# Performance work log

Measured on AMD Instinct MI355X. Metric: run time of the kernel, lower is better.

Reference implementation:

```python
import jax, jax.numpy as jnp
import numpy as np

HEADS = 4
HID = 610
KER = 50  # cov2KerSize
NEG_SLOPE = 0.2


def gat_layer(x, src, dst, w, b, att_src, att_dst, n_nodes):
    # x: [N, Fin], w: [HEADS*HID, Fin], att_*: [1, HEADS, HID], b: [HID]
    h = (x @ w.T).reshape(n_nodes, HEADS, HID)               # [N,H,D]
    a_src = (h * att_src).sum(-1)                            # [N,H]
    a_dst = (h * att_dst).sum(-1)                            # [N,H]
    alpha = jax.nn.leaky_relu(a_src[src] + a_dst[dst], NEG_SLOPE)  # [E,H]
    # softmax over edges grouped by destination node
    m = jax.ops.segment_max(alpha, dst, num_segments=n_nodes)
    e = jnp.exp(alpha - m[dst])
    denom = jax.ops.segment_sum(e, dst, num_segments=n_nodes)
    a = e / (denom[dst] + 1e-16)                             # [E,H]
    msg = h[src] * a[:, :, None]                             # [E,H,D]
    out = jax.ops.segment_sum(msg, dst, num_segments=n_nodes)  # [N,H,D]
    return out.mean(axis=1) + b                              # [N,D] (concat=False)


def setup_inputs() -> dict:
    key = jax.random.key(0)
    ks = jax.random.split(key, 16)
    N, E, FIN, NOUT = 20000, 100000, 128, 86
    x = jax.random.normal(ks[0], (N, FIN), dtype=jnp.float32)
    edge_index = jax.random.randint(ks[1], (2, E), 0, N, dtype=jnp.int64)
    def kaiming(k, shape, fan_in):
        return jax.random.normal(k, shape, dtype=jnp.float32) * np.float32(np.sqrt(2.0 / fan_in))
    w0 = kaiming(ks[2], (HEADS * HID, FIN), FIN)
    b0 = jnp.zeros((HID,), jnp.float32)
    att_src0 = kaiming(ks[3], (1, HEADS, HID), HID)
    att_dst0 = kaiming(ks[4], (1, HEADS, HID), HID)
    w2 = kaiming(ks[5], (HEADS * HID, HID), HID)
    b2 = jnp.zeros((HID,), jnp.float32)
    att_src1 = kaiming(ks[6], (1, HEADS, HID), HID)
    att_dst1 = kaiming(ks[7], (1, HEADS, HID), HID)
    w4 = kaiming(ks[8], (1, 1, 2, KER), 2 * KER)
    b4 = jnp.zeros((1,), jnp.float32)
    w6 = kaiming(ks[9], (1, 1, KER), KER)
    b6 = jnp.zeros((1,), jnp.float32)
    w8 = kaiming(ks[10], (NOUT, 512), 512)
    b8 = jnp.zeros((NOUT,), jnp.float32)
    return dict(x=x, edge_index=edge_index, w0=w0, b0=b0, att_src0=att_src0,
                att_dst0=att_dst0, w2=w2, b2=b2, att_src1=att_src1,
                att_dst1=att_dst1, w4=w4, b4=b4, w6=w6, b6=b6, w8=w8, b8=b8)


def reference(x, edge_index, w0, b0, att_src0, att_dst0, w2, b2, att_src1,
              att_dst1, w4, b4, w6, b6, w8, b8):
    N = x.shape[0]
    src, dst = edge_index[0], edge_index[1]
    x1 = jax.nn.relu(gat_layer(x, src, dst, w0, b0, att_src0, att_dst0, N))
    x2 = jax.nn.relu(gat_layer(x1, src, dst, w2, b2, att_src1, att_dst1, N))
    # edge features: cat(src_feat, dst_feat) viewed as [E,1,2,HID]
    ef = jnp.stack([x2[src], x2[dst]], axis=1)[:, None, :, :]  # [E,1,2,HID]
    y = jax.lax.conv_general_dilated(ef, w4, (1, 1), 'VALID',
                                     dimension_numbers=('NCHW', 'OIHW', 'NCHW'))
    y = jax.nn.relu(y + b4[None, :, None, None])               # [E,1,1,561]
    y = y.reshape(-1, HID - KER + 1, 1).transpose(0, 2, 1)     # [E,1,561]
    y = jax.lax.conv_general_dilated(y, w6, (1,), 'VALID',
                                     dimension_numbers=('NCH', 'OIH', 'NCH'))
    y = jax.nn.relu(y + b6[None, :, None])                     # [E,1,512]
    # adaptive_avg_pool1d to 512 is identity since length is already 512
    y = y.reshape(-1, 512)
    return y @ w8.T + b8                                       # [E, num_outputs]
```

## Files before the change

### kernel.cpp

```cpp
#include <hip/hip_runtime.h>
#include <math.h>

#define HEADS 4
#define HID 610
#define HIDP 640
#define FIN 128
#define KER 50
#define NOUT 86
#define NEG_SLOPE 0.2f

typedef short bf8_t __attribute__((ext_vector_type(8)));
typedef float f4_t __attribute__((ext_vector_type(4)));

__device__ __forceinline__ ushort f2bf(float f) {
    unsigned u = __float_as_uint(f);
    unsigned r = (u + 0x7FFFu + ((u >> 16) & 1u)) >> 16;
    return (ushort)r;
}
__device__ __forceinline__ float bf2f(ushort b) { return __uint_as_float(((unsigned)b) << 16); }

__global__ void fill_val(float* __restrict__ p, float v, long n) {
    long i = (long)blockIdx.x * blockDim.x + threadIdx.x;
    if (i < n) p[i] = v;
}

__global__ void copy_int(const int* __restrict__ a, int* __restrict__ b, int n) {
    int i = blockIdx.x * blockDim.x + threadIdx.x;
    if (i < n) b[i] = a[i];
}

__global__ void hist_k(const int* __restrict__ ei, int* __restrict__ hist, int E) {
    int e = blockIdx.x * blockDim.x + threadIdx.x;
    if (e < E) atomicAdd(&hist[ei[E + e]], 1);
}

__global__ __launch_bounds__(1024) void scan_k(const int* __restrict__ hist,
                                               int* __restrict__ base, int Nn) {
    __shared__ int tmp[1024];
    __shared__ int carry;
    if (threadIdx.x == 0) carry = 0;
    __syncthreads();
    for (int c0 = 0; c0 < Nn; c0 += 1024) {
        int i = c0 + threadIdx.x;
        int v = (i < Nn) ? hist[i] : 0;
        tmp[threadIdx.x] = v;
        __syncthreads();
        for (int off = 1; off < 1024; off <<= 1) {
            int t = (threadIdx.x >= off) ? tmp[threadIdx.x - off] : 0;
            __syncthreads();
            tmp[threadIdx.x] += t;
            __syncthreads();
        }
        if (i < Nn) base[i] = carry + tmp[threadIdx.x] - v;
        __syncthreads();
        if (threadIdx.x == 1023) carry += tmp[1023];
        __syncthreads();
    }
    if (threadIdx.x == 0) base[Nn] = carry;
}

__global__ void scatter_k(const int* __restrict__ ei, int* __restrict__ cursor,
                          int* __restrict__ esrc, int E) {
    int e = blockIdx.x * blockDim.x + threadIdx.x;
    if (e >= E) return;
    int d = ei[E + e];
    int pos = atomicAdd(&cursor[d], 1);
    esrc[pos] = ei[e];
}

__global__ void split_pad(const float* __restrict__ in, ushort* __restrict__ hi,
                          ushort* __restrict__ lo, int R, int K, int Kp) {
    long i = (long)blockIdx.x * blockDim.x + threadIdx.x;
    if (i >= (long)R * Kp) return;
    int r = (int)(i / Kp), c = (int)(i % Kp);
    float v = (c < K) ? in[(long)r * K + c] : 0.f;
    ushort h = f2bf(v);
    hi[i] = h;
    lo[i] = f2bf(v - bf2f(h));
}

template <int AMODE, bool BIAS>
__global__ __launch_bounds__(256) void gemm_mfma(const float* __restrict__ A,
                                                 const ushort* __restrict__ Aghi,
                                                 const ushort* __restrict__ Aglo,
                                                 const ushort* __restrict__ Bghi,
                                                 const ushort* __restrict__ Bglo,
                                                 const float* __restrict__ bias,
                                                 float* __restrict__ C,
                                                 int M, int N, int Kp) {
    __shared__ __align__(16) ushort Ah[128 * 32];
    __shared__ __align__(16) ushort Al[128 * 32];
    __shared__ __align__(16) ushort Bh[128 * 32];
    __shared__ __align__(16) ushort Bl[128 * 32];
    int tid = threadIdx.x;
    int wave = tid >> 6, lane = tid & 63;
    int quad = lane >> 4, l16 = lane & 15;
    int wm = wave & 1, wn = wave >> 1;
    int row0 = blockIdx.y * 128, col0 = blockIdx.x * 128;

    float4 pa0[4];
    uint4 pah[2], pal[2], pbh[2], pbl[2];

    auto loadA = [&](int k0) {
        if (AMODE == 0) {
#pragma unroll
            for (int q = 0; q < 4; q++) {
                int p = tid + q * 256;
                int r = p >> 3, c4 = (p & 7) << 2;
                int gr = row0 + r;
                pa0[q] = (gr < M) ? *(const float4*)(A + (size_t)gr * Kp + k0 + c4)
                                  : make_float4(0.f, 0.f, 0.f, 0.f);
            }
        } else {
#pragma unroll
            for (int q = 0; q < 2; q++) {
                int p = tid + q * 256;
                int r = p >> 2, c = p & 3;
                int gr = row0 + r;
                if (gr < M) {
                    pah[q] = *(const uint4*)(Aghi + (size_t)gr * Kp + k0 + c * 8);
                    pal[q] = *(const uint4*)(Aglo + (size_t)gr * Kp + k0 + c * 8);
                } else {
                    pah[q] = make_uint4(0, 0, 0, 0);
                    pal[q] = make_uint4(0, 0, 0, 0);
                }
            }
        }
    };
    auto loadB = [&](int k0) {
#pragma unroll
        for (int q = 0; q < 2; q++) {
            int p = tid + q * 256;
            int r = p >> 2, c = p & 3;
            int gr = col0 + r;
            if (gr < N) {
                pbh[q] = *(const uint4*)(Bghi + (size_t)gr * Kp + k0 + c * 8);
                pbl[q] = *(const uint4*)(Bglo + (size_t)gr * Kp + k0 + c * 8);
            } else {
                pbh[q] = make_uint4(0, 0, 0, 0);
                pbl[q] = make_uint4(0, 0, 0, 0);
            }
        }
    };
    auto writeLDS = [&]() {
        if (AMODE == 0) {
#pragma unroll
            for (int q = 0; q < 4; q++) {
                int p = tid + q * 256;
                int r = p >> 3, m = p & 7;
                int pos = r * 32 + ((((m >> 1)) ^ ((r >> 1) & 3)) << 3) + ((m & 1) << 2);
                float4 v = pa0[q];
                ushort4 hv, lv;
                hv.x = f2bf(v.x); lv.x = f2bf(v.x - bf2f(hv.x));
                hv.y = f2bf(v.y); lv.y = f2bf(v.y - bf2f(hv.y));
                hv.z = f2bf(v.z); lv.z = f2bf(v.z - bf2f(hv.z));
                hv.w = f2bf(v.w); lv.w = f2bf(v.w - bf2f(hv.w));
                *(ushort4*)&Ah[pos] = hv;
                *(ushort4*)&Al[pos] = lv;
            }
        } else {
#pragma unroll
            for (int q = 0; q < 2; q++) {
                int p = tid + q * 256;
                int r = p >> 2, c = p & 3;
                int pos = r * 32 + ((c ^ ((r >> 1) & 3)) << 3);
                *(uint4*)&Ah[pos] = pah[q];
                *(uint4*)&Al[pos] = pal[q];
            }
        }
#pragma unroll
        for (int q = 0; q < 2; q++) {
            int p = tid + q * 256;
            int r = p >> 2, c = p & 3;
            int pos = r * 32 + ((c ^ ((r >> 1) & 3)) << 3);
            *(uint4*)&Bh[pos] = pbh[q];
            *(uint4*)&Bl[pos] = pbl[q];
        }
    };

    f4_t acc[4][4];
#pragma unroll
    for (int i = 0; i < 4; i++)
#pragma unroll
        for (int j = 0; j < 4; j++) acc[i][j] = (f4_t){0.f, 0.f, 0.f, 0.f};

    loadA(0);
    loadB(0);
    int sw = (quad ^ ((l16 >> 1) & 3)) << 3;
    for (int k0 = 0; k0 < Kp; k0 += 32) {
        __syncthreads();
        writeLDS();
        __syncthreads();
        if (k0 + 32 < Kp) {
            loadA(k0 + 32);
            loadB(k0 + 32);
        }
        bf8_t ah[4], al[4], bh[4], bl[4];
#pragma unroll
        for (int t = 0; t < 4; t++) {
            int ar = wm * 64 + t * 16 + l16;
            ah[t] = *(const bf8_t*)&Ah[ar * 32 + sw];
            al[t] = *(const bf8_t*)&Al[ar * 32 + sw];
            int br = wn * 64 + t * 16 + l16;
            bh[t] = *(const bf8_t*)&Bh[br * 32 + sw];
            bl[t] = *(const bf8_t*)&Bl[br * 32 + sw];
        }
#pragma unroll
        for (int i = 0; i < 4; i++)
#pragma unroll
            for (int j = 0; j < 4; j++) {
                acc[i][j] = __builtin_amdgcn_mfma_f32_16x16x32_bf16(ah[i], bh[j], acc[i][j], 0, 0, 0);
                acc[i][j] = __builtin_amdgcn_mfma_f32_16x16x32_bf16(al[i], bh[j], acc[i][j], 0, 0, 0);
                acc[i][j] = __builtin_amdgcn_mfma_f32_16x16x32_bf16(ah[i], bl[j], acc[i][j], 0, 0, 0);
            }
    }
#pragma unroll
    for (int i = 0; i < 4; i++) {
#pragma unroll
        for (int r = 0; r < 4; r++) {
            int grow = row0 + wm * 64 + i * 16 + quad * 4 + r;
            if (grow >= M) continue;
#pragma unroll
            for (int j = 0; j < 4; j++) {
                int gcol = col0 + wn * 64 + j * 16 + l16;
                if (gcol >= N) continue;
                float v = acc[i][j][r];
                if (BIAS) v += bias[gcol];
                C[(size_t)grow * N + gcol] = v;
            }
        }
    }
}

__global__ __launch_bounds__(256) void attn_dots(const float* __restrict__ h,
                                                 const float* __restrict__ att_s,
                                                 const float* __restrict__ att_d,
                                                 float* __restrict__ a_src,
                                                 float* __restrict__ a_dst, int Nn) {
    int n = blockIdx.x;
    int head = threadIdx.x >> 6;
    int lane = threadIdx.x & 63;
    const float2* hr = (const float2*)(h + (long)n * (HEADS * HID) + head * HID);
    const float2* as = (const float2*)(att_s + head * HID);
    const float2* ad = (const float2*)(att_d + head * HID);
    float ss = 0.f, sd = 0.f;
    for (int d = lane; d < HID / 2; d += 64) {
        float2 hv = hr[d], av = as[d], dv = ad[d];
        ss += hv.x * av.x + hv.y * av.y;
        sd += hv.x * dv.x + hv.y * dv.y;
    }
    for (int off = 32; off > 0; off >>= 1) {
        ss += __shfl_down(ss, off);
        sd += __shfl_down(sd, off);
    }
    if (lane == 0) {
        a_src[n * HEADS + head] = ss;
        a_dst[n * HEADS + head] = sd;
    }
}

template <int OUTMODE>
__global__ __launch_bounds__(256) void node_aggregate(
    const float* __restrict__ h, const float* __restrict__ asrc,
    const float* __restrict__ adst, const int* __restrict__ base,
    const int* __restrict__ esrc, const float* __restrict__ bias,
    float* __restrict__ xout, ushort* __restrict__ xhi, ushort* __restrict__ xlo,
    int Nn) {
    int wave = threadIdx.x >> 6, lane = threadIdx.x & 63;
    int n = blockIdx.x * 4 + wave;
    if (n >= Nn) return;
    int b0 = base[n], deg = base[n + 1] - b0;
    float ad[HEADS];
#pragma unroll
    for (int hh = 0; hh < HEADS; hh++) ad[hh] = adst[n * HEADS + hh];
    float m[HEADS] = {-INFINITY, -INFINITY, -INFINITY, -INFINITY};
    for (int eb = 0; eb < deg; eb += 64) {
        int i = eb + lane;
        if (i < deg) {
            int s = esrc[b0 + i];
#pragma unroll
            for (int hh = 0; hh < HEADS; hh++) {
                float v = asrc[s * HEADS + hh] + ad[hh];
                v = v >= 0.f ? v : NEG_SLOPE * v;
                m[hh] = fmaxf(m[hh], v);
            }
        }
    }
#pragma unroll
    for (int off = 32; off > 0; off >>= 1)
#pragma unroll
        for (int hh = 0; hh < HEADS; hh++) m[hh] = fmaxf(m[hh], __shfl_xor(m[hh], off));
    float sden[HEADS] = {0.f, 0.f, 0.f, 0.f};
    for (int eb = 0; eb < deg; eb += 64) {
        int i = eb + lane;
        if (i < deg) {
            int s = esrc[b0 + i];
#pragma unroll
            for (int hh = 0; hh < HEADS; hh++) {
                float v = asrc[s * HEADS + hh] + ad[hh];
                v = v >= 0.f ? v : NEG_SLOPE * v;
                sden[hh] += expf(v - m[hh]);
            }
        }
    }
#pragma unroll
    for (int off = 32; off > 0; off >>= 1)
#pragma unroll
        for (int hh = 0; hh < HEADS; hh++) sden[hh] += __shfl_xor(sden[hh], off);
    float inv[HEADS];
#pragma unroll
    for (int hh = 0; hh < HEADS; hh++) inv[hh] = 0.25f / (sden[hh] + 1e-16f);
    float acc0[10] = {}, acc1[10] = {}, acc2[10] = {}, acc3[10] = {};
    for (int eb = 0; eb < deg; eb += 64) {
        int i = eb + lane;
        int sreg = 0;
        float coef[HEADS] = {0.f, 0.f, 0.f, 0.f};
        if (i < deg) {
            sreg = esrc[b0 + i];
#pragma unroll
            for (int hh = 0; hh < HEADS; hh++) {
                float v = asrc[sreg * HEADS + hh] + ad[hh];
                v = v >= 0.f ? v : NEG_SLOPE * v;
                coef[hh] = expf(v - m[hh]) * inv[hh];
            }
        }
        int cnt = deg - eb < 64 ? deg - eb : 64;
        for (int j = 0; j < cnt; j++) {
            int s = __shfl(sreg, j);
            float c0 = __shfl(coef[0], j), c1 = __shfl(coef[1], j);
            float c2 = __shfl(coef[2], j), c3 = __shfl(coef[3], j);
            const float* hr = h + (size_t)s * (HEADS * HID);
#pragma unroll
            for (int t = 0; t < 10; t++) {
                int d = lane + t * 64;
                if (d < HID) {
                    acc0[t] = fmaf(c0, hr[d], acc0[t]);
                    acc1[t] = fmaf(c1, hr[HID + d], acc1[t]);
                    acc2[t] = fmaf(c2, hr[2 * HID + d], acc2[t]);
                    acc3[t] = fmaf(c3, hr[3 * HID + d], acc3[t]);
                }
            }
        }
    }
#pragma unroll
    for (int t = 0; t < 10; t++) {
        int d = lane + t * 64;
        if (d < HID) {
            float v = acc0[t] + acc1[t] + acc2[t] + acc3[t] + bias[d];
            v = v > 0.f ? v : 0.f;
            if (OUTMODE == 0) {
                xout[(size_t)n * HIDP + d] = v;
            } else {
                ushort hv = f2bf(v);
                xhi[(size_t)n * HIDP + d] = hv;
                xlo[(size_t)n * HIDP + d] = f2bf(v - bf2f(hv));
            }
        }
    }
    for (int d = HID + lane; d < HIDP; d += 64) {
        if (OUTMODE == 0) {
            xout[(size_t)n * HIDP + d] = 0.f;
        } else {
            xhi[(size_t)n * HIDP + d] = 0;
            xlo[(size_t)n * HIDP + d] = 0;
        }
    }
}

__device__ __forceinline__ int ystag(int j) { return j + (j >> 3); }

__global__ __launch_bounds__(256) void edge_conv(const float* __restrict__ x2,
                                                 const int* __restrict__ ei,
                                                 const float* __restrict__ w4,
                                                 const float* __restrict__ b4,
                                                 const float* __restrict__ w6,
                                                 const float* __restrict__ b6,
                                                 ushort* __restrict__ zhi,
                                                 ushort* __restrict__ zlo, int E) {
    __shared__ __align__(16) float2 st[4][632];
    __shared__ __align__(16) float y[4][652];
    int wave = threadIdx.x >> 6;
    int lane = threadIdx.x & 63;
    int e = blockIdx.x * 4 + wave;
    bool active = (e < E);
    if (active) {
        int sidx = ei[e];
        int didx = ei[E + e];
        const float2* sp = (const float2*)(x2 + (long)sidx * HIDP);
        const float2* tp = (const float2*)(x2 + (long)didx * HIDP);
        for (int i = lane; i < HID / 2; i += 64) {
            float2 sv = sp[i], tv = tp[i];
            *(float4*)&st[wave][2 * i] = make_float4(sv.x, tv.x, sv.y, tv.y);
        }
    }
    __syncthreads();
    float bb4 = b4[0], bb6 = b6[0];
    if (active) {
        int j0 = lane * 9;
        float acc[9];
        float2 W[18];
#pragma unroll
        for (int i = 0; i < 9; i++) acc[i] = bb4;
#pragma unroll
        for (int p = 0; p < 18; p++) W[p] = st[wave][j0 + p];
#pragma unroll
        for (int g = 0; g < 6; g++) {
#pragma unroll
            for (int mm = 0; mm < 9; mm++) {
                int k = 9 * g + mm;
                if (k < KER) {
                    float ws_ = w4[k], wt_ = w4[KER + k];
#pragma unroll
                    for (int i = 0; i < 9; i++) {
                        float2 v = W[(9 * g + mm + i) % 18];
                        acc[i] = fmaf(v.x, ws_, acc[i]);
                        acc[i] = fmaf(v.y, wt_, acc[i]);
                    }
                }
            }
            if (g < 5) {
#pragma unroll
                for (int p = 0; p < 9; p++)
                    W[(9 * g + p) % 18] = st[wave][j0 + 9 * g + 18 + p];
            }
        }
#pragma unroll
        for (int i = 0; i < 9; i++)
            y[wave][ystag(j0 + i)] = acc[i] > 0.f ? acc[i] : 0.f;
    }
    __syncthreads();
    if (active) {
        int j0 = lane * 8;
        float acc[8];
        float Y[16];
#pragma unroll
        for (int i = 0; i < 8; i++) acc[i] = bb6;
#pragma unroll
        for (int p = 0; p < 16; p++) Y[p] = y[wave][ystag(j0 + p)];
#pragma unroll
        for (int g = 0; g < 7; g++) {
#pragma unroll
            for (int mm = 0; mm < 8; mm++) {
                int k = 8 * g + mm;
                if (k < KER) {
                    float wv = w6[k];
#pragma unroll
                    for (int i = 0; i < 8; i++)
                        acc[i] = fmaf(Y[(8 * g + mm + i) % 16], wv, acc[i]);
                }
            }
            if (g < 6) {
#pragma unroll
                for (int p = 0; p < 8; p++)
                    Y[(8 * g + p) % 16] = y[wave][ystag(j0 + 8 * g + 16 + p)];
            }
        }
        ushort4 zh0, zh1, zl0, zl1;
        float v;
        v = acc[0] > 0.f ? acc[0] : 0.f; zh0.x = f2bf(v); zl0.x = f2bf(v - bf2f(zh0.x));
        v = acc[1] > 0.f ? acc[1] : 0.f; zh0.y = f2bf(v); zl0.y = f2bf(v - bf2f(zh0.y));
        v = acc[2] > 0.f ? acc[2] : 0.f; zh0.z = f2bf(v); zl0.z = f2bf(v - bf2f(zh0.z));
        v = acc[3] > 0.f ? acc[3] : 0.f; zh0.w = f2bf(v); zl0.w = f2bf(v - bf2f(zh0.w));
        v = acc[4] > 0.f ? acc[4] : 0.f; zh1.x = f2bf(v); zl1.x = f2bf(v - bf2f(zh1.x));
        v = acc[5] > 0.f ? acc[5] : 0.f; zh1.y = f2bf(v); zl1.y = f2bf(v - bf2f(zh1.y));
        v = acc[6] > 0.f ? acc[6] : 0.f; zh1.z = f2bf(v); zl1.z = f2bf(v - bf2f(zh1.z));
        v = acc[7] > 0.f ? acc[7] : 0.f; zh1.w = f2bf(v); zl1.w = f2bf(v - bf2f(zh1.w));
        size_t zo = (size_t)e * 512 + j0;
        *(ushort4*)&zhi[zo] = zh0;
        *(ushort4*)&zhi[zo + 4] = zh1;
        *(ushort4*)&zlo[zo] = zl0;
        *(ushort4*)&zlo[zo + 4] = zl1;
    }
}

extern "C" void kernel_launch(void* const* d_in, const int* in_sizes, int n_in,
                              void* d_out, int out_size, void* d_ws, size_t ws_size,
                              hipStream_t stream) {
    const float* x = (const float*)d_in[0];
    const int* ei = (const int*)d_in[1];
    const float* w0 = (const float*)d_in[2];
    const float* b0 = (const float*)d_in[3];
    const float* att_s0 = (const float*)d_in[4];
    const float* att_d0 = (const float*)d_in[5];
    const float* w2 = (const float*)d_in[6];
    const float* b2 = (const float*)d_in[7];
    const float* att_s1 = (const float*)d_in[8];
    const float* att_d1 = (const float*)d_in[9];
    const float* w4 = (const float*)d_in[10];
    const float* b4 = (const float*)d_in[11];
    const float* w6 = (const float*)d_in[12];
    const float* b6 = (const float*)d_in[13];
    const float* w8 = (const float*)d_in[14];
    const float* b8 = (const float*)d_in[15];
    float* out = (float*)d_out;

    const int Nn = in_sizes[0] / FIN;
    const int E = in_sizes[1] / 2;
    const int HD = HEADS * HID;

    float* ws = (float*)d_ws;
    size_t o = 0;
    float* buf1 = ws + o; o += (size_t)Nn * HIDP;
    ushort* x1hi = (ushort*)buf1;
    ushort* x1lo = x1hi + (size_t)Nn * HIDP;
    ushort* w8hi = (ushort*)(ws + o);
    ushort* w8lo = w8hi + (size_t)NOUT * 512; o += (size_t)NOUT * 512;
    ushort* zhi = (ushort*)(ws + o);
    ushort* zlo = zhi + (size_t)E * 512;
    int* base = (int*)(ws + o); o += (size_t)Nn + 4;
    int* cursor = (int*)(ws + o); o += (size_t)Nn;
    int* esrc = (int*)(ws + o); o += (size_t)E;
    float* asrc = ws + o; o += (size_t)Nn * HEADS;
    float* adst = ws + o; o += (size_t)Nn * HEADS;
    ushort* w0hi = (ushort*)(ws + o);
    ushort* w0lo = w0hi + (size_t)HD * FIN; o += (size_t)HD * FIN;
    ushort* w2hi = (ushort*)(ws + o);
    ushort* w2lo = w2hi + (size_t)HD * HIDP; o += (size_t)HD * HIDP;
    float* h = ws + o;

    int edgeGrid = (E + 255) / 256;
    int nodeWaveGrid = (Nn + 3) / 4;
    int edgeConvGrid = (E + 3) / 4;
    dim3 gGemmL((HD + 127) / 128, (Nn + 127) / 128);
    dim3 gGemmF((NOUT + 127) / 128, (E + 127) / 128);

    split_pad<<<((HD * FIN) + 255) / 256, 256, 0, stream>>>(w0, w0hi, w0lo, HD, FIN, FIN);
    split_pad<<<((HD * HIDP) + 255) / 256, 256, 0, stream>>>(w2, w2hi, w2lo, HD, HID, HIDP);
    split_pad<<<((NOUT * 512) + 255) / 256, 256, 0, stream>>>(w8, w8hi, w8lo, NOUT, 512, 512);
    fill_val<<<(Nn + 255) / 256, 256, 0, stream>>>((float*)cursor, 0.f, Nn);
    hist_k<<<edgeGrid, 256, 0, stream>>>(ei, cursor, E);
    scan_k<<<1, 1024, 0, stream>>>(cursor, base, Nn);
    copy_int<<<(Nn + 255) / 256, 256, 0, stream>>>(base, cursor, Nn);
    scatter_k<<<edgeGrid, 256, 0, stream>>>(ei, cursor, esrc, E);

    gemm_mfma<0, false><<<gGemmL, 256, 0, stream>>>(x, nullptr, nullptr, w0hi, w0lo, nullptr,
                                                    h, Nn, HD, FIN);
    attn_dots<<<Nn, 256, 0, stream>>>(h, att_s0, att_d0, asrc, adst, Nn);
    node_aggregate<1><<<nodeWaveGrid, 256, 0, stream>>>(h, asrc, adst, base, esrc, b0,
                                                        nullptr, x1hi, x1lo, Nn);

    gemm_mfma<1, false><<<gGemmL, 256, 0, stream>>>(nullptr, x1hi, x1lo, w2hi, w2lo, nullptr,
                                                    h, Nn, HD, HIDP);
    attn_dots<<<Nn, 256, 0, stream>>>(h, att_s1, att_d1, asrc, adst, Nn);
    node_aggregate<0><<<nodeWaveGrid, 256, 0, stream>>>(h, asrc, adst, base, esrc, b2,
                                                        buf1, nullptr, nullptr, Nn);

    edge_conv<<<edgeConvGrid, 256, 0, stream>>>(buf1, ei, w4, b4, w6, b6, zhi, zlo, E);

    gemm_mfma<1, true><<<gGemmF, 256, 0, stream>>>(nullptr, zhi, zlo, w8hi, w8lo, b8,
                                                   out, E, NOUT, 512);
}
```

Before: 1.124 ms.

## Fold attention vectors into weights and vectorize node aggregation loads

Precomputes U = W^T·att per head so the attention logits come from a small GEMV on the layer input (x or x1) rather than a pass over the full h tensor. This removes the read of the large N×2440 h matrix in each attention-dot kernel. Node aggregation also switches to float2 loads and stores. The reassociated dot product changes floating-point rounding slightly, and compute_u runs serial per-thread loops over HID.

Result: slower. 1.210 ms (+7.6%).

```diff
diff --git a/kernel.cpp b/kernel.cpp
--- a/kernel.cpp
+++ b/kernel.cpp
@@ -77,6 +77,22 @@
     ushort h = f2bf(v);
     hi[i] = h;
     lo[i] = f2bf(v - bf2f(h));
+}
+
+__global__ void compute_u(const float* __restrict__ w, const float* __restrict__ att_s,
+                          const float* __restrict__ att_d, float* __restrict__ U,
+                          int K, int Kp) {
+    int gid = blockIdx.x * blockDim.x + threadIdx.x;
+    if (gid >= Kp * 8) return;
+    int k = gid % Kp, c = gid / Kp;
+    int h = c & 3;
+    const float* att = (c < 4) ? att_s : att_d;
+    float acc = 0.f;
+    if (k < K) {
+        for (int d = 0; d < HID; d++)
+            acc += w[((size_t)(h * HID + d)) * K + k] * att[h * HID + d];
+    }
+    U[k * 8 + c] = acc;
 }
 
 template <int AMODE, bool BIAS>
@@ -232,30 +248,74 @@
     }
 }
 
-__global__ __launch_bounds__(256) void attn_dots(const float* __restrict__ h,
-                                                 const float* __restrict__ att_s,
-                                                 const float* __restrict__ att_d,
-                                                 float* __restrict__ a_src,
-                                                 float* __restrict__ a_dst, int Nn) {
-    int n = blockIdx.x;
-    int head = threadIdx.x >> 6;
-    int lane = threadIdx.x & 63;
-    const float2* hr = (const float2*)(h + (long)n * (HEADS * HID) + head * HID);
-    const float2* as = (const float2*)(att_s + head * HID);
-    const float2* ad = (const float2*)(att_d + head * HID);
-    float ss = 0.f, sd = 0.f;
-    for (int d = lane; d < HID / 2; d += 64) {
-        float2 hv = hr[d], av = as[d], dv = ad[d];
-        ss += hv.x * av.x + hv.y * av.y;
-        sd += hv.x * dv.x + hv.y * dv.y;
-    }
-    for (int off = 32; off > 0; off >>= 1) {
-        ss += __shfl_down(ss, off);
-        sd += __shfl_down(sd, off);
-    }
+__global__ __launch_bounds__(256) void attn_gemv_f32(const float* __restrict__ x,
+                                                     const float* __restrict__ Ug,
+                                                     float* __restrict__ a_src,
+                                                     float* __restrict__ a_dst, int Nn) {
+    __shared__ float Us[FIN * 9];
+    for (int idx = threadIdx.x; idx < FIN * 8; idx += 256) {
+        int k = idx >> 3, c = idx & 7;
+        Us[k * 9 + c] = Ug[idx];
+    }
+    __syncthreads();
+    int wave = threadIdx.x >> 6, lane = threadIdx.x & 63;
+    int n = blockIdx.x * 4 + wave;
+    if (n >= Nn) return;
+    float acc[8] = {};
+#pragma unroll
+    for (int t = 0; t < 2; t++) {
+        int k = lane + 64 * t;
+        float v = x[(size_t)n * FIN + k];
+#pragma unroll
+        for (int c = 0; c < 8; c++) acc[c] = fmaf(v, Us[k * 9 + c], acc[c]);
+    }
+#pragma unroll
+    for (int off = 32; off > 0; off >>= 1)
+#pragma unroll
+        for (int c = 0; c < 8; c++) acc[c] += __shfl_xor(acc[c], off);
     if (lane == 0) {
-        a_src[n * HEADS + head] = ss;
-        a_dst[n * HEADS + head] = sd;
+#pragma unroll
+        for (int hh = 0; hh < 4; hh++) {
+            a_src[n * HEADS + hh] = acc[hh];
+            a_dst[n * HEADS + hh] = acc[4 + hh];
+        }
+    }
+}
+
+__global__ __launch_bounds__(256) void attn_gemv_bf(const ushort* __restrict__ xhi,
+                                                    const ushort* __restrict__ xlo,
+                                                    const float* __restrict__ Ug,
+                                                    float* __restrict__ a_src,
+                                                    float* __restrict__ a_dst, int Nn) {
+    __shared__ float Us[HIDP * 9];
+    for (int idx = threadIdx.x; idx < HIDP * 8; idx += 256) {
+        int k = idx >> 3, c = idx & 7;
+        Us[k * 9 + c] = Ug[idx];
+    }
+    __syncthreads();
+    int wave = threadIdx.x >> 6, lane = threadIdx.x & 63;
+    int n = blockIdx.x * 4 + wave;
+    if (n >= Nn) return;
+    const ushort* hp = xhi + (size_t)n * HIDP;
+    const ushort* lp = xlo + (size_t)n * HIDP;
+    float acc[8] = {};
+#pragma unroll
+    for (int t = 0; t < 10; t++) {
+        int k = lane + 64 * t;
+        float v = bf2f(hp[k]) + bf2f(lp[k]);
+#pragma unroll
+        for (int c = 0; c < 8; c++) acc[c] = fmaf(v, Us[k * 9 + c], acc[c]);
+    }
+#pragma unroll
+    for (int off = 32; off > 0; off >>= 1)
+#pragma unroll
+        for (int c = 0; c < 8; c++) acc[c] += __shfl_xor(acc[c], off);
+    if (lane == 0) {
+#pragma unroll
+        for (int hh = 0; hh < 4; hh++) {
+            a_src[n * HEADS + hh] = acc[hh];
+            a_dst[n * HEADS + hh] = acc[4 + hh];
+        }
     }
 }
 
@@ -310,7 +370,12 @@
     float inv[HEADS];
 #pragma unroll
     for (int hh = 0; hh < HEADS; hh++) inv[hh] = 0.25f / (sden[hh] + 1e-16f);
-    float acc0[10] = {}, acc1[10] = {}, acc2[10] = {}, acc3[10] = {};
+    float2 a0[5], a1[5], a2[5], a3[5];
+#pragma unroll
+    for (int t = 0; t < 5; t++) {
+        a0[t] = make_float2(0.f, 0.f); a1[t] = make_float2(0.f, 0.f);
+        a2[t] = make_float2(0.f, 0.f); a3[t] = make_float2(0.f, 0.f);
+    }
     for (int eb = 0; eb < deg; eb += 64) {
         int i = eb + lane;
         int sreg = 0;
@@ -329,31 +394,41 @@
             int s = __shfl(sreg, j);
             float c0 = __shfl(coef[0], j), c1 = __shfl(coef[1], j);
             float c2 = __shfl(coef[2], j), c3 = __shfl(coef[3], j);
-            const float* hr = h + (size_t)s * (HEADS * HID);
-#pragma unroll
-            for (int t = 0; t < 10; t++) {
-                int d = lane + t * 64;
-                if (d < HID) {
-                    acc0[t] = fmaf(c0, hr[d], acc0[t]);
-                    acc1[t] = fmaf(c1, hr[HID + d], acc1[t]);
-                    acc2[t] = fmaf(c2, hr[2 * HID + d], acc2[t]);
-                    acc3[t] = fmaf(c3, hr[3 * HID + d], acc3[t]);
+            const float2* hr2 = (const float2*)(h + (size_t)s * (HEADS * HID));
+#pragma unroll
+            for (int t = 0; t < 5; t++) {
+                int f = lane + t * 64;
+                if (f < 305) {
+                    float2 v0 = hr2[f];
+                    float2 v1 = hr2[305 + f];
+                    float2 v2 = hr2[610 + f];
+                    float2 v3 = hr2[915 + f];
+                    a0[t].x = fmaf(c0, v0.x, a0[t].x); a0[t].y = fmaf(c0, v0.y, a0[t].y);
+                    a1[t].x = fmaf(c1, v1.x, a1[t].x); a1[t].y = fmaf(c1, v1.y, a1[t].y);
+                    a2[t].x = fmaf(c2, v2.x, a2[t].x); a2[t].y = fmaf(c2, v2.y, a2[t].y);
+                    a3[t].x = fmaf(c3, v3.x, a3[t].x); a3[t].y = fmaf(c3, v3.y, a3[t].y);
                 }
             }
         }
     }
-#pragma unroll
-    for (int t = 0; t < 10; t++) {
-        int d = lane + t * 64;
-        if (d < HID) {
-            float v = acc0[t] + acc1[t] + acc2[t] + acc3[t] + bias[d];
-            v = v > 0.f ? v : 0.f;
+    const float2* b2p = (const float2*)bias;
+#pragma unroll
+    for (int t = 0; t < 5; t++) {
+        int f = lane + t * 64;
+        if (f < 305) {
+            float2 bv = b2p[f];
+            float vx = a0[t].x + a1[t].x + a2[t].x + a3[t].x + bv.x;
+            float vy = a0[t].y + a1[t].y + a2[t].y + a3[t].y + bv.y;
+            vx = vx > 0.f ? vx : 0.f;
+            vy = vy > 0.f ? vy : 0.f;
             if (OUTMODE == 0) {
-                xout[(size_t)n * HIDP + d] = v;
+                *(float2*)&xout[(size_t)n * HIDP + 2 * f] = make_float2(vx, vy);
             } else {
-                ushort hv = f2bf(v);
-                xhi[(size_t)n * HIDP + d] = hv;
-                xlo[(size_t)n * HIDP + d] = f2bf(v - bf2f(hv));
+                ushort2 hv, lv;
+                hv.x = f2bf(vx); lv.x = f2bf(vx - bf2f(hv.x));
+                hv.y = f2bf(vy); lv.y = f2bf(vy - bf2f(hv.y));
+                *(ushort2*)&xhi[(size_t)n * HIDP + 2 * f] = hv;
+                *(ushort2*)&xlo[(size_t)n * HIDP + 2 * f] = lv;
             }
         }
     }
@@ -512,6 +587,8 @@
     int* esrc = (int*)(ws + o); o += (size_t)E;
     float* asrc = ws + o; o += (size_t)Nn * HEADS;
     float* adst = ws + o; o += (size_t)Nn * HEADS;
+    float* U0 = ws + o; o += (size_t)FIN * 8;
+    float* U2 = ws + o; o += (size_t)HIDP * 8;
     ushort* w0hi = (ushort*)(ws + o);
     ushort* w0lo = w0hi + (size_t)HD * FIN; o += (size_t)HD * FIN;
     ushort* w2hi = (ushort*)(ws + o);
@@ -527,6 +604,8 @@
     split_pad<<<((HD * FIN) + 255) / 256, 256, 0, stream>>>(w0, w0hi, w0lo, HD, FIN, FIN);
     split_pad<<<((HD * HIDP) + 255) / 256, 256, 0, stream>>>(w2, w2hi, w2lo, HD, HID, HIDP);
     split_pad<<<((NOUT * 512) + 255) / 256, 256, 0, stream>>>(w8, w8hi, w8lo, NOUT, 512, 512);
+    compute_u<<<(FIN * 8 + 255) / 256, 256, 0, stream>>>(w0, att_s0, att_d0, U0, FIN, FIN);
+    compute_u<<<(HIDP * 8 + 255) / 256, 256, 0, stream>>>(w2, att_s1, att_d1, U2, HID, HIDP);
     fill_val<<<(Nn + 255) / 256, 256, 0, stream>>>((float*)cursor, 0.f, Nn);
     hist_k<<<edgeGrid, 256, 0, stream>>>(ei, cursor, E);
     scan_k<<<1, 1024, 0, stream>>>(cursor, base, Nn);
@@ -535,13 +614,13 @@
 
     gemm_mfma<0, false><<<gGemmL, 256, 0, stream>>>(x, nullptr, nullptr, w0hi, w0lo, nullptr,
                                                     h, Nn, HD, FIN);
-    attn_dots<<<Nn, 256, 0, stream>>>(h, att_s0, att_d0, asrc, adst, Nn);
+    attn_gemv_f32<<<nodeWaveGrid, 256, 0, stream>>>(x, U0, asrc, adst, Nn);
     node_aggregate<1><<<nodeWaveGrid, 256, 0, stream>>>(h, asrc, adst, base, esrc, b0,
                                                         nullptr, x1hi, x1lo, Nn);
 
     gemm_mfma<1, false><<<gGemmL, 256, 0, stream>>>(nullptr, x1hi, x1lo, w2hi, w2lo, nullptr,
                                                     h, Nn, HD, HIDP);
-    attn_dots<<<Nn, 256, 0, stream>>>(h, att_s1, att_d1, asrc, adst, Nn);
+    attn_gemv_bf<<<nodeWaveGrid, 256, 0, stream>>>(x1hi, x1lo, U2, asrc, adst, Nn);
     node_aggregate<0><<<nodeWaveGrid, 256, 0, stream>>>(h, asrc, adst, base, esrc, b2,
                                                         buf1, nullptr, nullptr, Nn);
 
```
